# Kernel tuning notes

Hardware: AMD Instinct MI355X
Metric: run time of the kernel (lower is better)

The kernel has to match this reference:

```python
import jax, jax.numpy as jnp
import numpy as np
from jax import lax


def grouped_linear(x, w):
    # x: [d0, d1, G*ws], w: [G, ws, out_per_group] -> [d0, d1, G*out_per_group]
    d0, d1, _ = x.shape
    G, ws, o = w.shape
    x = x.reshape(d0, d1, G, ws)
    return jnp.einsum('btgi,gio->btgh'.replace('h', 'o'), x, w).reshape(d0, d1, G * o)


def gru_layer(x, w_ih, w_hh, b_ih, b_hh):
    # x: [T, H_in]; w_ih/w_hh: [3, H, H_in]; b_ih/b_hh: [3, H]; gate order (r, z, n)
    ih = jnp.einsum('ti,ghi->tgh', x, w_ih) + b_ih  # input projections for all t at once

    def step(h, ih_t):
        hh = jnp.einsum('i,ghi->gh', h, w_hh) + b_hh
        r = jax.nn.sigmoid(ih_t[0] + hh[0])
        z = jax.nn.sigmoid(ih_t[1] + hh[1])
        n = jnp.tanh(ih_t[2] + r * hh[2])
        h_new = n + z * (h - n)
        return h_new, h_new

    h0 = jnp.zeros((w_hh.shape[1],), x.dtype)
    _, ys = lax.scan(step, h0, ih)
    return ys  # [T, H]


def setup_inputs() -> dict:
    key = jax.random.key(0)
    T, B, H = 8192, 1, 512
    HID, G, L = 512, 8, 2
    C_IN, C_OUT, F, KT = 64, 10, 96, 2
    ks = jax.random.split(key, 17)
    s = jnp.float32(0.05)
    return {
        'emb_tbh': jax.random.normal(ks[0], (T, B, H), jnp.float32),
        'c0': jax.random.normal(ks[1], (B, C_IN, T, F), jnp.float32),
        'lin_in_w': jax.random.normal(ks[2], (G, H // G, HID // G), jnp.float32) * s,
        'gru_w_ih': jax.random.normal(ks[3], (L, 3, HID, HID), jnp.float32) * s,
        'gru_w_hh': jax.random.normal(ks[4], (L, 3, HID, HID), jnp.float32) * s,
        'gru_b_ih': jax.random.normal(ks[5], (L, 3, HID), jnp.float32) * s,
        'gru_b_hh': jax.random.normal(ks[6], (L, 3, HID), jnp.float32) * s,
        'gru_skip_w': jax.random.normal(ks[7], (HID, HID), jnp.float32) * s,
        'gru_skip_b': jax.random.normal(ks[8], (HID,), jnp.float32) * s,
        'lin_out_w': jax.random.normal(ks[9], (G, HID // G, HID // G), jnp.float32) * s,
        'df_skip_w': jax.random.normal(ks[10], (HID, H), jnp.float32) * s,
        'df_skip_b': jax.random.normal(ks[11], (HID,), jnp.float32) * s,
        'fc_a_w': jax.random.normal(ks[12], (1, HID), jnp.float32) * s,
        'fc_a_b': jax.random.normal(ks[13], (1,), jnp.float32) * s,
        'df_out_w': jax.random.normal(ks[14], (G, HID // G, (F * C_OUT) // G), jnp.float32) * s,
        'convp_w': jax.random.normal(ks[15], (C_OUT, C_IN, KT, 1), jnp.float32) * s,
        'convp_b': jax.random.normal(ks[16], (C_OUT,), jnp.float32) * s,
    }


def reference(emb_tbh, c0, lin_in_w, gru_w_ih, gru_w_hh, gru_b_ih, gru_b_hh,
              gru_skip_w, gru_skip_b, lin_out_w, df_skip_w, df_skip_b,
              fc_a_w, fc_a_b, df_out_w, convp_w, convp_b):
    T, B, H = emb_tbh.shape  # B == 1 (manual GRU loop assumes it)
    DF_BINS, DF_OUT_CH = 96, 10

    # --- squeezed GRU: grouped linear_in + ReLU, manual GRU layers, skip, grouped linear_out + ReLU
    x = jax.nn.relu(grouped_linear(emb_tbh, lin_in_w))  # [T, B, HID]
    gru_in = x
    h = x[:, 0, :]  # [T, HID], B == 1
    for l in range(gru_w_ih.shape[0]):
        h = gru_layer(h, gru_w_ih[l], gru_w_hh[l], gru_b_ih[l], gru_b_hh[l])
    x = h[:, None, :]
    x = x + (gru_in @ gru_skip_w.T + gru_skip_b)
    x = jax.nn.relu(grouped_linear(x, lin_out_w))  # [T, B, HID]

    # --- skip from embedding + alpha head
    emb = emb_tbh.reshape(B, T, H)  # B==1: pure relabel of dims
    c = x.reshape(B, T, -1)
    c = c + (emb @ df_skip_w.T + df_skip_b)
    alpha = jax.nn.sigmoid(c @ fc_a_w.T + fc_a_b)  # [B, T, 1]

    # --- df_convp: causal time pad (top=1) + Conv2d kernel (2,1), then permute to [B,T,F,Cout]
    c0p = jnp.pad(c0, ((0, 0), (0, 0), (1, 0), (0, 0)))
    c0c = lax.conv_general_dilated(c0p, convp_w, (1, 1), 'VALID',
                                   dimension_numbers=('NCHW', 'OIHW', 'NCHW'))
    c0c = c0c + convp_b[None, :, None, None]
    c0c = jnp.transpose(c0c, (0, 2, 3, 1))  # [B, T, F, Cout]

    # --- df_out: grouped linear + tanh, reshape to coef grid, add conv pathway
    c = jnp.tanh(grouped_linear(c, df_out_w))  # [B, T, F*Cout]
    c = c.reshape(B, T, DF_BINS, DF_OUT_CH) + c0c
    return (c, alpha)
```

## Files before the change

kernel.cpp:

```cpp
#include <hip/hip_runtime.h>
#include <hip/hip_bf16.h>
#include <cstdint>

#define T_STEPS 8192
#define NWG3 64

typedef unsigned long long ull;

__device__ __forceinline__ float fast_sigmoid(float v) {
  return __fdividef(1.f, 1.f + __expf(-v));
}
__device__ __forceinline__ float fast_tanh(float v) {
  return 1.f - __fdividef(2.f, __expf(2.f * v) + 1.f);
}

__device__ __forceinline__ ull packpair(float v, unsigned tag) {
  return ((ull)__float_as_uint(v) << 32) | (ull)tag;
}

__device__ __forceinline__ void acc4(float& acc, const float4& wv, const float4& hv) {
  acc = fmaf(hv.x, wv.x, acc); acc = fmaf(hv.y, wv.y, acc);
  acc = fmaf(hv.z, wv.z, acc); acc = fmaf(hv.w, wv.w, acc);
}

__device__ __forceinline__ void pin4(float4& v) {
  asm volatile("" : "+v"(v.x), "+v"(v.y), "+v"(v.z), "+v"(v.w));
}

__global__ __launch_bounds__(256) void k_grouped_relu(const float* __restrict__ in,
                                                      const float* __restrict__ W,
                                                      float* __restrict__ out) {
  __shared__ float es[512];
  const int t = blockIdx.x;
  const int tid = threadIdx.x;
  const float* inr = in + (size_t)t * 512;
  ((float2*)es)[tid] = ((const float2*)inr)[tid];
  __syncthreads();
#pragma unroll
  for (int rep = 0; rep < 2; ++rep) {
    int jj = tid + rep * 256;
    int g = jj >> 6, o = jj & 63;
    const float* wp = W + (g << 12) + o;
    const float* ep = es + (g << 6);
    float acc = 0.f;
#pragma unroll 8
    for (int i = 0; i < 64; ++i) acc = fmaf(ep[i], wp[i << 6], acc);
    out[(size_t)t * 512 + jj] = fmaxf(acc, 0.f);
  }
}

__global__ __launch_bounds__(256) void k_gemm_rr(const float* __restrict__ A,
                                                 const float* __restrict__ B,
                                                 const float* __restrict__ bias,
                                                 const float* __restrict__ add,
                                                 float* __restrict__ C, int N) {
  __shared__ float As[64][68];
  __shared__ float Bs[64][68];
  const int bm = blockIdx.x << 6, bn = blockIdx.y << 6;
  const int tid = threadIdx.x;
  const int tx = tid & 15, ty = tid >> 4;
  float acc[4][4] = {};
  for (int k0 = 0; k0 < 512; k0 += 64) {
#pragma unroll
    for (int u = 0; u < 4; ++u) {
      int f4 = (u << 8) + tid;
      int m = f4 >> 4;
      int kq = (f4 & 15) << 2;
      float4 av = *(const float4*)(A + (size_t)(bm + m) * 512 + k0 + kq);
      As[kq + 0][m] = av.x; As[kq + 1][m] = av.y; As[kq + 2][m] = av.z; As[kq + 3][m] = av.w;
      float4 bv = *(const float4*)(B + (size_t)(bn + m) * 512 + k0 + kq);
      Bs[kq + 0][m] = bv.x; Bs[kq + 1][m] = bv.y; Bs[kq + 2][m] = bv.z; Bs[kq + 3][m] = bv.w;
    }
    __syncthreads();
#pragma unroll
    for (int k = 0; k < 64; ++k) {
      float4 a4 = *(const float4*)(&As[k][ty << 2]);
      float4 b4 = *(const float4*)(&Bs[k][tx << 2]);
      float ar[4] = {a4.x, a4.y, a4.z, a4.w};
      float br[4] = {b4.x, b4.y, b4.z, b4.w};
#pragma unroll
      for (int i = 0; i < 4; ++i)
#pragma unroll
        for (int j = 0; j < 4; ++j) acc[i][j] = fmaf(ar[i], br[j], acc[i][j]);
    }
    __syncthreads();
  }
  const int n0 = bn + (tx << 2);
  float4 bsv = *(const float4*)(bias + n0);
#pragma unroll
  for (int i = 0; i < 4; ++i) {
    int m = bm + (ty << 2) + i;
    float4 res;
    res.x = acc[i][0] + bsv.x; res.y = acc[i][1] + bsv.y;
    res.z = acc[i][2] + bsv.z; res.w = acc[i][3] + bsv.w;
    if (add) {
      float4 ad = *(const float4*)(add + (size_t)m * N + n0);
      res.x += ad.x; res.y += ad.y; res.z += ad.z; res.w += ad.w;
    }
    *(float4*)(C + (size_t)m * N + n0) = res;
  }
}

__global__ __launch_bounds__(512, 1) void k_gru_fused(
    const float* __restrict__ ih0,
    const float* __restrict__ Whh0, const float* __restrict__ bhh0,
    const float* __restrict__ Wih1, const float* __restrict__ bih1,
    const float* __restrict__ Whh1, const float* __restrict__ bhh1,
    float* __restrict__ h1seq,
    ull* __restrict__ ring0,
    ull* __restrict__ ring1) {
  __shared__ float h0s[2][512];
  __shared__ float h1s[2][512];
  const int wg = blockIdx.x, tid = threadIdx.x;
  const int w = tid >> 6, l = tid & 63;
  const int r = (wg << 3) + w;
  const bool pollH1 = (w >= 4);
  const int pidx = ((w & 3) << 6) + l;

  float4 W9[9][2];
#pragma unroll
  for (int g = 0; g < 3; ++g) {
    size_t off = ((size_t)g << 18) + ((size_t)r << 9) + ((size_t)l << 3);
    W9[g][0]     = *(const float4*)(Whh0 + off); W9[g][1]     = *(const float4*)(Whh0 + off + 4);
    W9[3 + g][0] = *(const float4*)(Wih1 + off); W9[3 + g][1] = *(const float4*)(Wih1 + off + 4);
    W9[6 + g][0] = *(const float4*)(Whh1 + off); W9[6 + g][1] = *(const float4*)(Whh1 + off + 4);
  }
#pragma unroll
  for (int i = 0; i < 9; ++i) { pin4(W9[i][0]); pin4(W9[i][1]); }
  float b9[9] = {};
  if (l == 0) {
#pragma unroll
    for (int g = 0; g < 3; ++g) {
      b9[g] = bhh0[(g << 9) + r];
      b9[3 + g] = bih1[(g << 9) + r];
      b9[6 + g] = bhh1[(g << 9) + r];
    }
  }
#pragma unroll
  for (int i = 0; i < 9; ++i) asm volatile("" : "+v"(b9[i]));
  float h0own = 0.f, h1own = 0.f;

  for (int t = 0; t <= T_STEPS; ++t) {
    float i0 = 0.f, i1 = 0.f, i2 = 0.f;
    if (l == 0 && t < T_STEPS) {
      const float* p = ih0 + (size_t)t * 1536 + r;
      i0 = p[0]; i1 = p[512]; i2 = p[1024];
    }
    {
      ull* sp = pollH1 ? (ring1 + ((t & 1) << 9)) : (ring0 + (((t + 1) & 1) << 9));
      const unsigned expm = pollH1 ? (unsigned)((t > 0) ? t - 1 : 0) : (unsigned)t;
      ull Pa, Pb;
      for (;;) {
        Pa = __hip_atomic_load(sp + pidx, __ATOMIC_RELAXED, __HIP_MEMORY_SCOPE_AGENT);
        Pb = __hip_atomic_load(sp + pidx + 256, __ATOMIC_RELAXED, __HIP_MEMORY_SCOPE_AGENT);
        bool bad = (((unsigned)Pa) != expm) | (((unsigned)Pb) != expm);
        if (__ballot(bad) == 0ull) break;
      }
      float* dst = pollH1 ? h1s[t & 1] : h0s[t & 1];
      dst[pidx] = __uint_as_float((unsigned)(Pa >> 32));
      dst[pidx + 256] = __uint_as_float((unsigned)(Pb >> 32));
    }
    __syncthreads();
    float4 h0a = *(const float4*)(&h0s[t & 1][l << 3]);
    float4 h0b = *(const float4*)(&h0s[t & 1][(l << 3) + 4]);
    float4 h1a = *(const float4*)(&h1s[t & 1][l << 3]);
    float4 h1b = *(const float4*)(&h1s[t & 1][(l << 3) + 4]);
    float acc[9];
#pragma unroll
    for (int i = 0; i < 9; ++i) acc[i] = 0.f;
#pragma unroll
    for (int i = 0; i < 6; ++i) { acc4(acc[i], W9[i][0], h0a); acc4(acc[i], W9[i][1], h0b); }
#pragma unroll
    for (int i = 6; i < 9; ++i) { acc4(acc[i], W9[i][0], h1a); acc4(acc[i], W9[i][1], h1b); }
#pragma unroll
    for (int m = 1; m < 64; m <<= 1)
#pragma unroll
      for (int i = 0; i < 9; ++i) acc[i] += __shfl_xor(acc[i], m);
    if (l == 0) {
      if (t < T_STEPS) {
        float rr = fast_sigmoid(i0 + acc[0] + b9[0]);
        float zz = fast_sigmoid(i1 + acc[1] + b9[1]);
        float nn = fast_tanh(fmaf(rr, acc[2] + b9[2], i2));
        h0own = fmaf(zz, h0own - nn, nn);
        __hip_atomic_store(ring0 + ((t & 1) << 9) + r, packpair(h0own, (unsigned)(t + 1)),
                           __ATOMIC_RELAXED, __HIP_MEMORY_SCOPE_AGENT);
      }
      if (t >= 1) {
        float rr = fast_sigmoid(acc[3] + b9[3] + acc[6] + b9[6]);
        float zz = fast_sigmoid(acc[4] + b9[4] + acc[7] + b9[7]);
        float nn = fast_tanh(fmaf(rr, acc[8] + b9[8], acc[5] + b9[5]));
        h1own = fmaf(zz, h1own - nn, nn);
        __hip_atomic_store(ring1 + (((t + 1) & 1) << 9) + r, packpair(h1own, (unsigned)t),
                           __ATOMIC_RELAXED, __HIP_MEMORY_SCOPE_AGENT);
        h1seq[(size_t)(t - 1) * 512 + r] = h1own;
      }
    }
  }
}

__global__ __launch_bounds__(256) void k_alpha(const float* __restrict__ c,
                                               const float* __restrict__ w,
                                               const float* __restrict__ b,
                                               float* __restrict__ alpha) {
  const int wave = threadIdx.x >> 6, lane = threadIdx.x & 63;
  const int t = (blockIdx.x << 2) + wave;
  const float* cr = c + (size_t)t * 512;
  float acc = 0.f;
#pragma unroll
  for (int q = 0; q < 8; ++q) acc = fmaf(cr[lane + (q << 6)], w[lane + (q << 6)], acc);
#pragma unroll
  for (int m = 32; m; m >>= 1) acc += __shfl_xor(acc, m);
  if (lane == 0) alpha[t] = 1.f / (1.f + __expf(-(acc + b[0])));
}

__global__ __launch_bounds__(256) void k_dfout_conv(const float* __restrict__ c,
                                                    const float* __restrict__ Wd,
                                                    const float* __restrict__ c0,
                                                    const float* __restrict__ wc,
                                                    const float* __restrict__ bc,
                                                    float* __restrict__ out) {
  __shared__ float cs[512];
  __shared__ float A0[64 * 96];
  __shared__ float A1[64 * 96];
  __shared__ float wcs[1280];
  __shared__ float cc[960];
  const int t = blockIdx.x, tid = threadIdx.x;
  ((float2*)cs)[tid] = ((const float2*)(c + (size_t)t * 512))[tid];
  for (int idx = tid; idx < 64 * 96; idx += 256) {
    int ci = idx / 96, f = idx - ci * 96;
    size_t base = (size_t)ci * ((size_t)T_STEPS * 96) + (size_t)t * 96 + f;
    A1[idx] = c0[base];
    A0[idx] = (t == 0) ? 0.f : c0[base - 96];
  }
  for (int idx = tid; idx < 1280; idx += 256) wcs[idx] = wc[idx];
  __syncthreads();
  for (int idx = tid; idx < 960; idx += 256) {
    int f = idx / 10, co = idx - f * 10;
    float acc = bc[co];
    const float* w = wcs + (co << 7);
#pragma unroll 16
    for (int ci = 0; ci < 64; ++ci) {
      acc = fmaf(A0[ci * 96 + f], w[ci * 2 + 0], acc);
      acc = fmaf(A1[ci * 96 + f], w[ci * 2 + 1], acc);
    }
    cc[idx] = acc;
  }
  __syncthreads();
  for (int idx = tid; idx < 960; idx += 256) {
    int g = idx / 120, o = idx - g * 120;
    const float* wp = Wd + g * 7680 + o;
    const float* ep = cs + (g << 6);
    float acc = 0.f;
#pragma unroll 16
    for (int i = 0; i < 64; ++i) acc = fmaf(ep[i], wp[i * 120], acc);
    out[(size_t)t * 960 + idx] = tanhf(acc) + cc[idx];
  }
}

extern "C" void kernel_launch(void* const* d_in, const int* in_sizes, int n_in,
                              void* d_out, int out_size, void* d_ws, size_t ws_size,
                              hipStream_t stream) {
  const float* emb       = (const float*)d_in[0];
  const float* c0        = (const float*)d_in[1];
  const float* lin_in_w  = (const float*)d_in[2];
  const float* w_ih      = (const float*)d_in[3];
  const float* w_hh      = (const float*)d_in[4];
  const float* b_ih      = (const float*)d_in[5];
  const float* b_hh      = (const float*)d_in[6];
  const float* skip_w    = (const float*)d_in[7];
  const float* skip_b    = (const float*)d_in[8];
  const float* lin_out_w = (const float*)d_in[9];
  const float* df_skip_w = (const float*)d_in[10];
  const float* df_skip_b = (const float*)d_in[11];
  const float* fc_a_w    = (const float*)d_in[12];
  const float* fc_a_b    = (const float*)d_in[13];
  const float* df_out_w  = (const float*)d_in[14];
  const float* convp_w   = (const float*)d_in[15];
  const float* convp_b   = (const float*)d_in[16];

  const size_t T = T_STEPS;
  float* x    = (float*)d_ws;
  float* ih   = x + T * 512;
  float* h1   = ih + T * 1536;
  ull* ring0  = (ull*)(h1 + T * 512);
  ull* ring1  = ring0 + 1024;
  float* sbuf = ih;
  float* vbuf = ih + T * 512;
  float* cbuf = ih + 2 * T * 512;
  float* outc = (float*)d_out;
  float* outa = outc + T * 960;

  k_grouped_relu<<<T_STEPS, 256, 0, stream>>>(emb, lin_in_w, x);
  k_gemm_rr<<<dim3(128, 24), 256, 0, stream>>>(x, w_ih, b_ih, nullptr, ih, 1536);
  (void)hipMemsetAsync(ring0, 0, 2048 * sizeof(ull), stream);
  k_gru_fused<<<NWG3, 512, 0, stream>>>(ih, w_hh, b_hh,
                                        w_ih + 786432, b_ih + 1536,
                                        w_hh + 786432, b_hh + 1536,
                                        h1, ring0, ring1);
  k_gemm_rr<<<dim3(128, 8), 256, 0, stream>>>(x, skip_w, skip_b, h1, sbuf, 512);
  k_grouped_relu<<<T_STEPS, 256, 0, stream>>>(sbuf, lin_out_w, vbuf);
  k_gemm_rr<<<dim3(128, 8), 256, 0, stream>>>(emb, df_skip_w, df_skip_b, vbuf, cbuf, 512);
  k_alpha<<<T_STEPS / 4, 256, 0, stream>>>(cbuf, fc_a_w, fc_a_b, outa);
  k_dfout_conv<<<T_STEPS, 256, 0, stream>>>(cbuf, df_out_w, c0, convp_w, convp_b, outc);
  (void)in_sizes; (void)n_in; (void)out_size; (void)ws_size;
}
```

Baseline: 34.67 ms.

## Spread fused GRU over 128 workgroups with shared-memory weights and vectorized polling

The persistent fused two-layer GRU kernel now runs 128 workgroups of 256 threads (4 rows each) instead of 64 of 512, so more CUs share the serial recurrence. Recurrent weights move from pinned registers into LDS. Each thread now polls four contiguous ring entries, and h vectors are staged as float4 in LDS. The aim is a shorter per-step critical path through less work per workgroup and fewer pollers per WG. The cost is more workgroups in the cross-WG spin synchronization and extra LDS reads of the weights every step.

```diff
diff --git a/kernel.cpp b/kernel.cpp
--- a/kernel.cpp
+++ b/kernel.cpp
@@ -3,7 +3,7 @@
 #include <cstdint>
 
 #define T_STEPS 8192
-#define NWG3 64
+#define NWG4 128
 
 typedef unsigned long long ull;
 
@@ -18,13 +18,10 @@
   return ((ull)__float_as_uint(v) << 32) | (ull)tag;
 }
 
-__device__ __forceinline__ void acc4(float& acc, const float4& wv, const float4& hv) {
-  acc = fmaf(hv.x, wv.x, acc); acc = fmaf(hv.y, wv.y, acc);
-  acc = fmaf(hv.z, wv.z, acc); acc = fmaf(hv.w, wv.w, acc);
-}
-
-__device__ __forceinline__ void pin4(float4& v) {
-  asm volatile("" : "+v"(v.x), "+v"(v.y), "+v"(v.z), "+v"(v.w));
+__device__ __forceinline__ float dot4(const float4& a, const float4& b) {
+  float s = a.x * b.x;
+  s = fmaf(a.y, b.y, s); s = fmaf(a.z, b.z, s); s = fmaf(a.w, b.w, s);
+  return s;
 }
 
 __global__ __launch_bounds__(256) void k_grouped_relu(const float* __restrict__ in,
@@ -101,7 +98,7 @@
   }
 }
 
-__global__ __launch_bounds__(512, 1) void k_gru_fused(
+__global__ __launch_bounds__(256, 1) void k_gru_fused(
     const float* __restrict__ ih0,
     const float* __restrict__ Whh0, const float* __restrict__ bhh0,
     const float* __restrict__ Wih1, const float* __restrict__ bih1,
@@ -109,24 +106,24 @@
     float* __restrict__ h1seq,
     ull* __restrict__ ring0,
     ull* __restrict__ ring1) {
-  __shared__ float h0s[2][512];
-  __shared__ float h1s[2][512];
+  __shared__ float4 wl[4][9][2][64];
+  __shared__ float4 hb[2][2][2][64];
   const int wg = blockIdx.x, tid = threadIdx.x;
   const int w = tid >> 6, l = tid & 63;
-  const int r = (wg << 3) + w;
-  const bool pollH1 = (w >= 4);
-  const int pidx = ((w & 3) << 6) + l;
-
-  float4 W9[9][2];
-#pragma unroll
-  for (int g = 0; g < 3; ++g) {
-    size_t off = ((size_t)g << 18) + ((size_t)r << 9) + ((size_t)l << 3);
-    W9[g][0]     = *(const float4*)(Whh0 + off); W9[g][1]     = *(const float4*)(Whh0 + off + 4);
-    W9[3 + g][0] = *(const float4*)(Wih1 + off); W9[3 + g][1] = *(const float4*)(Wih1 + off + 4);
-    W9[6 + g][0] = *(const float4*)(Whh1 + off); W9[6 + g][1] = *(const float4*)(Whh1 + off + 4);
-  }
-#pragma unroll
-  for (int i = 0; i < 9; ++i) { pin4(W9[i][0]); pin4(W9[i][1]); }
+  const int base = wg << 2;
+  const int r = base + w;
+
+  for (int idx = tid; idx < 4 * 9 * 2 * 64; idx += 256) {
+    const int ll = idx & 63;
+    const int p = (idx >> 6) & 1;
+    const int rest = idx >> 7;
+    const int gi = rest % 9;
+    const int rr = rest / 9;
+    const int m = gi / 3, g = gi - m * 3;
+    const float* srcm = (m == 0) ? Whh0 : ((m == 1) ? Wih1 : Whh1);
+    const size_t off = ((size_t)g << 18) + ((size_t)(base + rr) << 9) + (ll << 3) + (p << 2);
+    wl[rr][gi][p][ll] = *(const float4*)(srcm + off);
+  }
   float b9[9] = {};
   if (l == 0) {
 #pragma unroll
@@ -136,8 +133,10 @@
       b9[6 + g] = bhh1[(g << 9) + r];
     }
   }
-#pragma unroll
-  for (int i = 0; i < 9; ++i) asm volatile("" : "+v"(b9[i]));
+  __syncthreads();
+
+  const int vec = tid >> 7;
+  const int tt = tid & 127;
   float h0own = 0.f, h1own = 0.f;
 
   for (int t = 0; t <= T_STEPS; ++t) {
@@ -147,31 +146,38 @@
       i0 = p[0]; i1 = p[512]; i2 = p[1024];
     }
     {
-      ull* sp = pollH1 ? (ring1 + ((t & 1) << 9)) : (ring0 + (((t + 1) & 1) << 9));
-      const unsigned expm = pollH1 ? (unsigned)((t > 0) ? t - 1 : 0) : (unsigned)t;
-      ull Pa, Pb;
+      ull* sp = vec ? (ring1 + ((t & 1) << 9)) : (ring0 + (((t + 1) & 1) << 9));
+      const unsigned expm = vec ? (unsigned)((t > 0) ? t - 1 : 0) : (unsigned)t;
+      const int e0 = tt << 2;
+      ull P0, P1, P2, P3;
       for (;;) {
-        Pa = __hip_atomic_load(sp + pidx, __ATOMIC_RELAXED, __HIP_MEMORY_SCOPE_AGENT);
-        Pb = __hip_atomic_load(sp + pidx + 256, __ATOMIC_RELAXED, __HIP_MEMORY_SCOPE_AGENT);
-        bool bad = (((unsigned)Pa) != expm) | (((unsigned)Pb) != expm);
-        if (__ballot(bad) == 0ull) break;
+        P0 = __hip_atomic_load(sp + e0 + 0, __ATOMIC_RELAXED, __HIP_MEMORY_SCOPE_AGENT);
+        P1 = __hip_atomic_load(sp + e0 + 1, __ATOMIC_RELAXED, __HIP_MEMORY_SCOPE_AGENT);
+        P2 = __hip_atomic_load(sp + e0 + 2, __ATOMIC_RELAXED, __HIP_MEMORY_SCOPE_AGENT);
+        P3 = __hip_atomic_load(sp + e0 + 3, __ATOMIC_RELAXED, __HIP_MEMORY_SCOPE_AGENT);
+        unsigned bad = (((unsigned)P0) ^ expm) | (((unsigned)P1) ^ expm) |
+                       (((unsigned)P2) ^ expm) | (((unsigned)P3) ^ expm);
+        if (__ballot(bad != 0) == 0ull) break;
       }
-      float* dst = pollH1 ? h1s[t & 1] : h0s[t & 1];
-      dst[pidx] = __uint_as_float((unsigned)(Pa >> 32));
-      dst[pidx + 256] = __uint_as_float((unsigned)(Pb >> 32));
+      float4 v;
+      v.x = __uint_as_float((unsigned)(P0 >> 32));
+      v.y = __uint_as_float((unsigned)(P1 >> 32));
+      v.z = __uint_as_float((unsigned)(P2 >> 32));
+      v.w = __uint_as_float((unsigned)(P3 >> 32));
+      hb[t & 1][vec][tt & 1][tt >> 1] = v;
     }
     __syncthreads();
-    float4 h0a = *(const float4*)(&h0s[t & 1][l << 3]);
-    float4 h0b = *(const float4*)(&h0s[t & 1][(l << 3) + 4]);
-    float4 h1a = *(const float4*)(&h1s[t & 1][l << 3]);
-    float4 h1b = *(const float4*)(&h1s[t & 1][(l << 3) + 4]);
+    float4 h0a = hb[t & 1][0][0][l];
+    float4 h0b = hb[t & 1][0][1][l];
+    float4 h1a = hb[t & 1][1][0][l];
+    float4 h1b = hb[t & 1][1][1][l];
     float acc[9];
 #pragma unroll
-    for (int i = 0; i < 9; ++i) acc[i] = 0.f;
-#pragma unroll
-    for (int i = 0; i < 6; ++i) { acc4(acc[i], W9[i][0], h0a); acc4(acc[i], W9[i][1], h0b); }
-#pragma unroll
-    for (int i = 6; i < 9; ++i) { acc4(acc[i], W9[i][0], h1a); acc4(acc[i], W9[i][1], h1b); }
+    for (int i = 0; i < 6; ++i)
+      acc[i] = dot4(wl[w][i][0][l], h0a) + dot4(wl[w][i][1][l], h0b);
+#pragma unroll
+    for (int i = 6; i < 9; ++i)
+      acc[i] = dot4(wl[w][i][0][l], h1a) + dot4(wl[w][i][1][l], h1b);
 #pragma unroll
     for (int m = 1; m < 64; m <<= 1)
 #pragma unroll
@@ -293,7 +299,7 @@
   k_grouped_relu<<<T_STEPS, 256, 0, stream>>>(emb, lin_in_w, x);
   k_gemm_rr<<<dim3(128, 24), 256, 0, stream>>>(x, w_ih, b_ih, nullptr, ih, 1536);
   (void)hipMemsetAsync(ring0, 0, 2048 * sizeof(ull), stream);
-  k_gru_fused<<<NWG3, 512, 0, stream>>>(ih, w_hh, b_hh,
+  k_gru_fused<<<NWG4, 256, 0, stream>>>(ih, w_hh, b_hh,
                                         w_ih + 786432, b_ih + 1536,
                                         w_hh + 786432, b_hh + 1536,
                                         h1, ring0, ring1);
```

Result: slower. 46.61 ms (+34.4%).
